# Kernel tuning notes

Hardware: AMD Instinct MI355X
Metric: run time of the kernel (lower is better)

## Reference

```python
import jax, jax.numpy as jnp
import numpy as np

VOCAB, D, PAD, SPARSITY = 6, 32, 5, 0.15


def setup_inputs() -> dict:
    key = jax.random.key(0)
    ks = jax.random.split(key, 16)
    x = jax.random.randint(ks[0], (256, 4096), 0, VOCAB, dtype=jnp.int32)
    s = 0.1
    emb = jax.random.normal(ks[1], (VOCAB, D), jnp.float32) * s
    return {
        "x": x,
        "emb": emb,
        # selector: D -> D//2 -> 1 (sigmoid)
        "sel_w1": jax.random.normal(ks[2], (D, D // 2), jnp.float32) * s,
        "sel_b1": jnp.zeros((D // 2,), jnp.float32),
        "sel_w2": jax.random.normal(ks[3], (D // 2, 1), jnp.float32) * s,
        "sel_b2": jnp.zeros((1,), jnp.float32),
        # approximator: D -> D -> D
        "app_w1": jax.random.normal(ks[4], (D, D), jnp.float32) * s,
        "app_b1": jnp.zeros((D,), jnp.float32),
        "app_w2": jax.random.normal(ks[5], (D, D), jnp.float32) * s,
        "app_b2": jnp.zeros((D,), jnp.float32),
        # classifier: D -> D//2 -> 1 (sigmoid)
        "cls_w1": jax.random.normal(ks[6], (D, D // 2), jnp.float32) * s,
        "cls_b1": jnp.zeros((D // 2,), jnp.float32),
        "cls_w2": jax.random.normal(ks[7], (D // 2, 1), jnp.float32) * s,
        "cls_b2": jnp.zeros((1,), jnp.float32),
    }


def reference(x, emb, sel_w1, sel_b1, sel_w2, sel_b2,
              app_w1, app_b1, app_w2, app_b2,
              cls_w1, cls_b1, cls_w2, cls_b2):
    B, S = x.shape
    k = max(1, int(S * SPARSITY))
    table = emb.at[PAD].set(0.0)            # padding_idx row is zero
    e = table[x]                            # [B, S, D]
    # selector scores (tiny MLP + sigmoid)
    h = jax.nn.relu(e @ sel_w1 + sel_b1)
    scores = jax.nn.sigmoid((h @ sel_w2 + sel_b2).squeeze(-1))  # [B, S]
    _, top_idx = jax.lax.top_k(scores, k)   # [B, k]
    sel = jnp.take_along_axis(e, top_idx[..., None], axis=1)    # [B, k, D]
    a = jax.nn.relu(sel @ app_w1 + app_b1) @ app_w2 + app_b2    # [B, k, D]
    pooled = a.mean(axis=1)                 # [B, D]
    c = jax.nn.relu(pooled @ cls_w1 + cls_b1)
    pred = jax.nn.sigmoid((c @ cls_w2 + cls_b2).squeeze(-1))    # [B]
    return pred, top_idx, scores
```

## Files before the change

kernel.cpp:

```cpp
#include <hip/hip_runtime.h>
#include <math.h>

#define VOCABN 6
#define DIM 32
#define PADI 5
#define BATCH 256
#define SEQ 4096
#define KSEL 614

__global__ __launch_bounds__(1024) void fused_row_kernel(
    const int* __restrict__ x,
    const float* __restrict__ emb,
    const float* __restrict__ sel_w1, const float* __restrict__ sel_b1,
    const float* __restrict__ sel_w2, const float* __restrict__ sel_b2,
    const float* __restrict__ app_w1, const float* __restrict__ app_b1,
    const float* __restrict__ app_w2, const float* __restrict__ app_b2,
    const float* __restrict__ cls_w1, const float* __restrict__ cls_b1,
    const float* __restrict__ cls_w2, const float* __restrict__ cls_b2,
    float* __restrict__ out_pred,
    float* __restrict__ out_topidx,
    float* __restrict__ out_scores) {
    const int b = blockIdx.x;
    const int t = threadIdx.x;
    const int lane = t & 63;
    const int w = t >> 6;

    __shared__ float s_emb[VOCABN * DIM];
    __shared__ float s_selw1[DIM * (DIM / 2)];
    __shared__ float s_selb1[DIM / 2], s_selw2[DIM / 2];
    __shared__ float s_appw1[DIM * DIM];
    __shared__ float s_appb1[DIM];
    __shared__ float s_appw2[DIM * DIM];
    __shared__ float s_appb2[DIM];
    __shared__ float s_clsw1[DIM * (DIM / 2)];
    __shared__ float s_clsb1[DIM / 2], s_clsw2[DIM / 2];
    __shared__ float s_selb2, s_clsb2v;
    __shared__ float s_ah[VOCABN * DIM];
    __shared__ float s_a[VOCABN * DIM];
    __shared__ float s_score[VOCABN];
    __shared__ int s_wtot[16][VOCABN];
    __shared__ int s_sel[VOCABN], s_base[VOCABN];
    __shared__ float s_pooled[DIM], s_c[DIM / 2];

    const int4 tw = *(const int4*)(x + (size_t)b * SEQ + t * 4);

    if (t < VOCABN * DIM) s_emb[t] = (t >= PADI * DIM) ? 0.f : emb[t];
    if (t < 512) s_selw1[t] = sel_w1[t];
    else if (t < 1024) s_clsw1[t - 512] = cls_w1[t - 512];
    s_appw1[t] = app_w1[t];
    s_appw2[t] = app_w2[t];
    if (t >= 192 && t < 208) { int i = t - 192; s_selb1[i] = sel_b1[i]; s_selw2[i] = sel_w2[i]; }
    else if (t >= 208 && t < 224) { int i = t - 208; s_clsb1[i] = cls_b1[i]; s_clsw2[i] = cls_w2[i]; }
    else if (t >= 224 && t < 256) { int i = t - 224; s_appb1[i] = app_b1[i]; s_appb2[i] = app_b2[i]; }
    else if (t == 256) s_selb2 = sel_b2[0];
    else if (t == 257) s_clsb2v = cls_b2[0];

    int tok[4];
    tok[0] = tw.x; tok[1] = tw.y; tok[2] = tw.z; tok[3] = tw.w;
    __syncthreads();

    if (t < 48) {
        const int v = t >> 3, j0 = (t & 7) * 2;
        float h0 = s_selb1[j0], h1 = s_selb1[j0 + 1];
        #pragma unroll
        for (int d = 0; d < DIM; ++d) {
            const float e = s_emb[v * DIM + d];
            h0 += e * s_selw1[d * (DIM / 2) + j0];
            h1 += e * s_selw1[d * (DIM / 2) + j0 + 1];
        }
        float part = fmaxf(h0, 0.f) * s_selw2[j0] + fmaxf(h1, 0.f) * s_selw2[j0 + 1];
        part += __shfl_xor(part, 1, 64);
        part += __shfl_xor(part, 2, 64);
        part += __shfl_xor(part, 4, 64);
        if ((t & 7) == 0) s_score[v] = 1.f / (1.f + expf(-(part + s_selb2)));
    } else if (t >= 128 && t < 128 + VOCABN * DIM) {
        const int i = t - 128, v = i >> 5, j = i & 31;
        float acc = s_appb1[j];
        #pragma unroll
        for (int d = 0; d < DIM; ++d) acc += s_emb[v * DIM + d] * s_appw1[d * DIM + j];
        s_ah[i] = fmaxf(acc, 0.f);
    }
    __syncthreads();

    if (t >= 128 && t < 128 + VOCABN * DIM) {
        const int i = t - 128, v = i >> 5, d = i & 31;
        float acc = s_appb2[d];
        #pragma unroll
        for (int j = 0; j < DIM; ++j) acc += s_ah[v * DIM + j] * s_appw2[j * DIM + d];
        s_a[i] = acc;
    }
    {
        float4 f;
        f.x = s_score[tok[0]]; f.y = s_score[tok[1]];
        f.z = s_score[tok[2]]; f.w = s_score[tok[3]];
        *(float4*)(out_scores + (size_t)b * SEQ + t * 4) = f;
    }

    int cnt[VOCABN], val[VOCABN];
    #pragma unroll
    for (int v = 0; v < VOCABN; ++v) {
        int c = 0;
        #pragma unroll
        for (int i = 0; i < 4; ++i) c += (tok[i] == v) ? 1 : 0;
        cnt[v] = c; val[v] = c;
    }
    for (int off = 1; off < 64; off <<= 1) {
        #pragma unroll
        for (int v = 0; v < VOCABN; ++v) {
            int up = __shfl_up(val[v], off, 64);
            if (lane >= off) val[v] += up;
        }
    }
    if (lane == 63) {
        #pragma unroll
        for (int v = 0; v < VOCABN; ++v) s_wtot[w][v] = val[v];
    }
    __syncthreads();

    int excl[VOCABN];
    #pragma unroll
    for (int v = 0; v < VOCABN; ++v) {
        int pre = 0;
        for (int ww = 0; ww < w; ++ww) pre += s_wtot[ww][v];
        excl[v] = pre + val[v] - cnt[v];
    }

    if (t == 0) {
        int rank[VOCABN];
        #pragma unroll
        for (int v = 0; v < VOCABN; ++v) {
            const float my = s_score[v];
            int r = 0;
            for (int u = 0; u < VOCABN; ++u) {
                if (s_score[u] > my) ++r;
                else if (s_score[u] == my && u < v) ++r;
            }
            rank[r] = v;
        }
        int rem = KSEL;
        for (int r = 0; r < VOCABN; ++r) {
            const int v = rank[r];
            int tot = 0;
            for (int ww = 0; ww < 16; ++ww) tot += s_wtot[ww][v];
            const int take = tot < rem ? tot : rem;
            s_base[v] = KSEL - rem;
            s_sel[v] = take;
            rem -= take;
        }
    }
    __syncthreads();

    #pragma unroll
    for (int v = 0; v < VOCABN; ++v) {
        int p = excl[v];
        const int sel = s_sel[v];
        const int bs = s_base[v];
        #pragma unroll
        for (int i = 0; i < 4; ++i) {
            if (tok[i] == v) {
                if (p < sel) out_topidx[(size_t)b * KSEL + bs + p] = (float)(t * 4 + i);
                ++p;
            }
        }
    }

    if (t < DIM) {
        float acc = 0.f;
        #pragma unroll
        for (int v = 0; v < VOCABN; ++v) acc += (float)s_sel[v] * s_a[v * DIM + t];
        s_pooled[t] = acc / (float)KSEL;
    }
    __syncthreads();
    if (t < DIM / 2) {
        float acc = s_clsb1[t];
        #pragma unroll
        for (int d = 0; d < DIM; ++d) acc += s_pooled[d] * s_clsw1[d * (DIM / 2) + t];
        s_c[t] = fmaxf(acc, 0.f);
    }
    __syncthreads();
    if (t == 0) {
        float z = s_clsb2v;
        #pragma unroll
        for (int j = 0; j < DIM / 2; ++j) z += s_c[j] * s_clsw2[j];
        out_pred[b] = 1.f / (1.f + expf(-z));
    }
}

extern "C" void kernel_launch(void* const* d_in, const int* in_sizes, int n_in,
                              void* d_out, int out_size, void* d_ws, size_t ws_size,
                              hipStream_t stream) {
    const int*   x      = (const int*)  d_in[0];
    const float* emb    = (const float*)d_in[1];
    const float* sel_w1 = (const float*)d_in[2];
    const float* sel_b1 = (const float*)d_in[3];
    const float* sel_w2 = (const float*)d_in[4];
    const float* sel_b2 = (const float*)d_in[5];
    const float* app_w1 = (const float*)d_in[6];
    const float* app_b1 = (const float*)d_in[7];
    const float* app_w2 = (const float*)d_in[8];
    const float* app_b2 = (const float*)d_in[9];
    const float* cls_w1 = (const float*)d_in[10];
    const float* cls_b1 = (const float*)d_in[11];
    const float* cls_w2 = (const float*)d_in[12];
    const float* cls_b2 = (const float*)d_in[13];

    float* out = (float*)d_out;
    float* out_pred   = out;
    float* out_topidx = out + BATCH;
    float* out_scores = out + BATCH + BATCH * KSEL;

    fused_row_kernel<<<BATCH, 1024, 0, stream>>>(
        x, emb, sel_w1, sel_b1, sel_w2, sel_b2,
        app_w1, app_b1, app_w2, app_b2,
        cls_w1, cls_b1, cls_w2, cls_b2,
        out_pred, out_topidx, out_scores);
}
```

Baseline: 90.14 us.

## Compute selector scores redundantly per wavefront and defer approximator MLP past barriers

Every wavefront now computes the six vocabulary selector scores itself, reading weights straight from global memory, and spreads them through lane shuffles and a register select chain instead of a shared-memory table. This removes the first block-wide barrier that sat between loading weights and writing the scores output, so the large score store can be issued earlier. The approximator's two MLP layers move later, overlapping the top-k bookkeeping, and one barrier is added between them. The cost is redundant selector arithmetic and global weight loads in all 16 wavefronts.

```diff
diff --git a/kernel.cpp b/kernel.cpp
--- a/kernel.cpp
+++ b/kernel.cpp
@@ -7,6 +7,17 @@
 #define BATCH 256
 #define SEQ 4096
 #define KSEL 614
+
+__device__ __forceinline__ float lut6(float s0, float s1, float s2, float s3,
+                                      float s4, float s5, int tk) {
+    float r = s0;
+    r = (tk == 1) ? s1 : r;
+    r = (tk == 2) ? s2 : r;
+    r = (tk == 3) ? s3 : r;
+    r = (tk == 4) ? s4 : r;
+    r = (tk == 5) ? s5 : r;
+    return r;
+}
 
 __global__ __launch_bounds__(1024) void fused_row_kernel(
     const int* __restrict__ x,
@@ -26,73 +37,69 @@
     const int w = t >> 6;
 
     __shared__ float s_emb[VOCABN * DIM];
-    __shared__ float s_selw1[DIM * (DIM / 2)];
-    __shared__ float s_selb1[DIM / 2], s_selw2[DIM / 2];
     __shared__ float s_appw1[DIM * DIM];
-    __shared__ float s_appb1[DIM];
     __shared__ float s_appw2[DIM * DIM];
-    __shared__ float s_appb2[DIM];
+    __shared__ float s_appb1[DIM], s_appb2[DIM];
     __shared__ float s_clsw1[DIM * (DIM / 2)];
     __shared__ float s_clsb1[DIM / 2], s_clsw2[DIM / 2];
-    __shared__ float s_selb2, s_clsb2v;
+    __shared__ float s_clsb2v;
     __shared__ float s_ah[VOCABN * DIM];
     __shared__ float s_a[VOCABN * DIM];
-    __shared__ float s_score[VOCABN];
     __shared__ int s_wtot[16][VOCABN];
     __shared__ int s_sel[VOCABN], s_base[VOCABN];
     __shared__ float s_pooled[DIM], s_c[DIM / 2];
 
     const int4 tw = *(const int4*)(x + (size_t)b * SEQ + t * 4);
 
-    if (t < VOCABN * DIM) s_emb[t] = (t >= PADI * DIM) ? 0.f : emb[t];
-    if (t < 512) s_selw1[t] = sel_w1[t];
-    else if (t < 1024) s_clsw1[t - 512] = cls_w1[t - 512];
     s_appw1[t] = app_w1[t];
     s_appw2[t] = app_w2[t];
-    if (t >= 192 && t < 208) { int i = t - 192; s_selb1[i] = sel_b1[i]; s_selw2[i] = sel_w2[i]; }
-    else if (t >= 208 && t < 224) { int i = t - 208; s_clsb1[i] = cls_b1[i]; s_clsw2[i] = cls_w2[i]; }
-    else if (t >= 224 && t < 256) { int i = t - 224; s_appb1[i] = app_b1[i]; s_appb2[i] = app_b2[i]; }
-    else if (t == 256) s_selb2 = sel_b2[0];
-    else if (t == 257) s_clsb2v = cls_b2[0];
+    if (t < 512) s_clsw1[t] = cls_w1[t];
+    else if (t < 704) { int i = t - 512; s_emb[i] = (i >= PADI * DIM) ? 0.f : emb[i]; }
+    else if (t < 736) { int i = t - 704; s_appb1[i] = app_b1[i]; }
+    else if (t < 768) { int i = t - 736; s_appb2[i] = app_b2[i]; }
+    else if (t < 784) { int i = t - 768; s_clsb1[i] = cls_b1[i]; }
+    else if (t < 800) { int i = t - 784; s_clsw2[i] = cls_w2[i]; }
+    else if (t == 800) s_clsb2v = cls_b2[0];
+
+    int sv = lane >> 3; if (sv >= VOCABN) sv -= VOCABN;
+    const int j0 = (lane & 7) * 2;
+    const float2 bj = *(const float2*)(sel_b1 + j0);
+    const float2 wj = *(const float2*)(sel_w2 + j0);
+    float h0 = bj.x, h1 = bj.y;
+    if (sv != PADI) {
+        const float4* e4 = (const float4*)(emb + sv * DIM);
+        #pragma unroll
+        for (int q = 0; q < 8; ++q) {
+            const float4 e = e4[q];
+            const float2 wa = *(const float2*)(sel_w1 + (q * 4 + 0) * (DIM / 2) + j0);
+            const float2 wb = *(const float2*)(sel_w1 + (q * 4 + 1) * (DIM / 2) + j0);
+            const float2 wc = *(const float2*)(sel_w1 + (q * 4 + 2) * (DIM / 2) + j0);
+            const float2 wd = *(const float2*)(sel_w1 + (q * 4 + 3) * (DIM / 2) + j0);
+            h0 += e.x * wa.x + e.y * wb.x + e.z * wc.x + e.w * wd.x;
+            h1 += e.x * wa.y + e.y * wb.y + e.z * wc.y + e.w * wd.y;
+        }
+    }
+    float part = fmaxf(h0, 0.f) * wj.x + fmaxf(h1, 0.f) * wj.y;
+    part += __shfl_xor(part, 1, 64);
+    part += __shfl_xor(part, 2, 64);
+    part += __shfl_xor(part, 4, 64);
+    const float sig = 1.f / (1.f + expf(-(part + sel_b2[0])));
+    const float sc0 = __shfl(sig,  0, 64);
+    const float sc1 = __shfl(sig,  8, 64);
+    const float sc2 = __shfl(sig, 16, 64);
+    const float sc3 = __shfl(sig, 24, 64);
+    const float sc4 = __shfl(sig, 32, 64);
+    const float sc5 = __shfl(sig, 40, 64);
 
     int tok[4];
     tok[0] = tw.x; tok[1] = tw.y; tok[2] = tw.z; tok[3] = tw.w;
-    __syncthreads();
-
-    if (t < 48) {
-        const int v = t >> 3, j0 = (t & 7) * 2;
-        float h0 = s_selb1[j0], h1 = s_selb1[j0 + 1];
-        #pragma unroll
-        for (int d = 0; d < DIM; ++d) {
-            const float e = s_emb[v * DIM + d];
-            h0 += e * s_selw1[d * (DIM / 2) + j0];
-            h1 += e * s_selw1[d * (DIM / 2) + j0 + 1];
-        }
-        float part = fmaxf(h0, 0.f) * s_selw2[j0] + fmaxf(h1, 0.f) * s_selw2[j0 + 1];
-        part += __shfl_xor(part, 1, 64);
-        part += __shfl_xor(part, 2, 64);
-        part += __shfl_xor(part, 4, 64);
-        if ((t & 7) == 0) s_score[v] = 1.f / (1.f + expf(-(part + s_selb2)));
-    } else if (t >= 128 && t < 128 + VOCABN * DIM) {
-        const int i = t - 128, v = i >> 5, j = i & 31;
-        float acc = s_appb1[j];
-        #pragma unroll
-        for (int d = 0; d < DIM; ++d) acc += s_emb[v * DIM + d] * s_appw1[d * DIM + j];
-        s_ah[i] = fmaxf(acc, 0.f);
-    }
-    __syncthreads();
-
-    if (t >= 128 && t < 128 + VOCABN * DIM) {
-        const int i = t - 128, v = i >> 5, d = i & 31;
-        float acc = s_appb2[d];
-        #pragma unroll
-        for (int j = 0; j < DIM; ++j) acc += s_ah[v * DIM + j] * s_appw2[j * DIM + d];
-        s_a[i] = acc;
-    }
+
     {
         float4 f;
-        f.x = s_score[tok[0]]; f.y = s_score[tok[1]];
-        f.z = s_score[tok[2]]; f.w = s_score[tok[3]];
+        f.x = lut6(sc0, sc1, sc2, sc3, sc4, sc5, tok[0]);
+        f.y = lut6(sc0, sc1, sc2, sc3, sc4, sc5, tok[1]);
+        f.z = lut6(sc0, sc1, sc2, sc3, sc4, sc5, tok[2]);
+        f.w = lut6(sc0, sc1, sc2, sc3, sc4, sc5, tok[3]);
         *(float4*)(out_scores + (size_t)b * SEQ + t * 4) = f;
     }
 
@@ -126,14 +133,14 @@
     }
 
     if (t == 0) {
+        float scv[VOCABN] = {sc0, sc1, sc2, sc3, sc4, sc5};
         int rank[VOCABN];
         #pragma unroll
         for (int v = 0; v < VOCABN; ++v) {
-            const float my = s_score[v];
             int r = 0;
             for (int u = 0; u < VOCABN; ++u) {
-                if (s_score[u] > my) ++r;
-                else if (s_score[u] == my && u < v) ++r;
+                if (scv[u] > scv[v]) ++r;
+                else if (scv[u] == scv[v] && u < v) ++r;
             }
             rank[r] = v;
         }
@@ -148,6 +155,13 @@
             rem -= take;
         }
     }
+    if (t >= 128 && t < 128 + VOCABN * DIM) {
+        const int i = t - 128, v = i >> 5, j = i & 31;
+        float acc = s_appb1[j];
+        #pragma unroll
+        for (int d = 0; d < DIM; ++d) acc += s_emb[v * DIM + d] * s_appw1[d * DIM + j];
+        s_ah[i] = fmaxf(acc, 0.f);
+    }
     __syncthreads();
 
     #pragma unroll
@@ -163,6 +177,15 @@
             }
         }
     }
+
+    if (t >= 128 && t < 128 + VOCABN * DIM) {
+        const int i = t - 128, v = i >> 5, d = i & 31;
+        float acc = s_appb2[d];
+        #pragma unroll
+        for (int j = 0; j < DIM; ++j) acc += s_ah[v * DIM + j] * s_appw2[j * DIM + d];
+        s_a[i] = acc;
+    }
+    __syncthreads();
 
     if (t < DIM) {
         float acc = 0.f;
```

Result: slower. 102.0 us (+13.1%).
